# Kernel tuning notes

Hardware: AMD Instinct MI355X
Metric: run time of the kernel (lower is better)

Reference implementation:

```python
import jax, jax.numpy as jnp
import numpy as np

KMEANS_ITERS = 3   # soft-kmeans refinement iterations
TOPK = 12          # hardcoded in the torch module
EPS = 1e-8


def _gather(x, idx):
    # batched_index_select: x (b, c, m); idx (b, n, k) -> (b, c, n, k)
    return jax.vmap(lambda xb, ib: xb[:, ib])(x, idx)


def _soft_kmeans(points, cent):
    # points (b, n, c); cent (b, m, c) -> refined centroids and soft assignment weights (b, n, m)
    for _ in range(KMEANS_ITERS):
        p2 = jnp.sum(points * points, axis=-1)           # (b, n)
        c2 = jnp.sum(cent * cent, axis=-1)               # (b, m)
        logits = -(p2[:, :, None] - 2.0 * jnp.einsum('bnc,bmc->bnm', points, cent) + c2[:, None, :])
        w = jax.nn.softmax(logits, axis=-1)              # (b, n, m)
        cent = jnp.einsum('bnm,bnc->bmc', w, points) / (jnp.sum(w, axis=1)[:, :, None] + EPS)
    return cent, w


def setup_inputs():
    key = jax.random.key(0)
    k1, k2, k3 = jax.random.split(key, 3)
    b, c, H, W, k = 4, 192, 80, 80, 9
    n = H * W
    out_c = 192
    x = jax.random.normal(k1, (b, c, n, 1), dtype=jnp.float32)
    edge_index = jax.random.randint(k2, (2, b, n, k), 0, n)
    conv_w = jax.random.normal(k3, (out_c, 3 * c), dtype=jnp.float32) * (1.0 / np.sqrt(3 * c))
    conv_b = jnp.zeros((out_c,), dtype=jnp.float32)
    return {"x": x, "edge_index": edge_index, "conv_w": conv_w, "conv_b": conv_b,
            "num_centroids": 50, "H": 80, "W": 80}


def reference(x, edge_index, conv_w, conv_b, num_centroids, H, W):
    b, c, n, _ = x.shape
    xs = x[..., 0]                                        # (b, c, n)
    # initial centroids: adaptive_avg_pool2d to (5, 10); H, W chosen divisible so bins are uniform
    x_img = xs.reshape(b, c, H, W)
    init_cent = x_img.reshape(b, c, 5, H // 5, 10, W // 10).mean(axis=(3, 5)).reshape(b, c, 50)
    # edge gathers + max-relative reduction
    x_i = _gather(xs, edge_index[1])                      # (b, c, n, k)
    x_j = _gather(xs, edge_index[0])                      # (b, c, n, k)
    x_j = jnp.max(x_j - x_i, axis=-1, keepdims=True)      # (b, c, n, 1)
    # soft-kmeans centroid construction
    points = jnp.transpose(xs, (0, 2, 1))                 # (b, n, c)
    cent, weights = _soft_kmeans(points, jnp.transpose(init_cent, (0, 2, 1)))
    cent = jnp.transpose(cent, (0, 2, 1))                 # (b, c, m)
    # topk centroid routing + second gather-max stage
    _, nn_idx = jax.lax.top_k(weights, TOPK)              # (b, n, 12)
    x_jc = _gather(cent, nn_idx)                          # (b, c, n, 12)
    x_jc = jnp.max(x_jc - xs[..., None], axis=-1, keepdims=True)  # (b, c, n, 1)
    # channel-interleaved concat (matches torch stack on dim=2 then reshape to 3c)
    feat = jnp.stack([x, x_j, x_jc], axis=2).reshape(b, 3 * c, n)  # (b, 3c, n)
    # BasicConv: 1x1 conv + bias + relu (norm=None)
    out = jnp.einsum('oi,bin->bon', conv_w, feat) + conv_b[None, :, None]
    return jax.nn.relu(out)[..., None]                    # (b, out_c, n, 1)
```

## Files before the change

kernel.cpp:

```cpp
#include <hip/hip_runtime.h>
#include <hip/hip_bf16.h>
#include <math.h>

#define B_   4
#define C_   192
#define N_   6400
#define K_   9
#define M_   50
#define TK_  12
#define OC_  192
#define KC_  576
#define CH_  100
#define LSTR 53
#define TSTR 72
#define XSTR 40
#define GSTR 40
#define GPB  8

typedef __bf16 b16x8 __attribute__((ext_vector_type(8)));
typedef float f32x4 __attribute__((ext_vector_type(4)));

__device__ inline unsigned short f2b(float f) {
    union { __hip_bfloat16 h; unsigned short u; } v;
    v.h = __float2bfloat16(f);
    return v.u;
}
__device__ inline float b2f(unsigned short u) {
    union { float f; unsigned int i; } v;
    v.i = ((unsigned int)u) << 16;
    return v.f;
}
__device__ inline void up8(uint4 v, float* f) {
    unsigned int w[4] = {v.x, v.y, v.z, v.w};
#pragma unroll
    for (int i = 0; i < 4; i++) {
        f[2 * i]     = b2f((unsigned short)(w[i] & 0xffffu));
        f[2 * i + 1] = b2f((unsigned short)(w[i] >> 16));
    }
}
__device__ inline uint4 pack8(const float* f) {
    unsigned int w[4];
#pragma unroll
    for (int i = 0; i < 4; i++)
        w[i] = (unsigned int)f2b(f[2 * i]) | ((unsigned int)f2b(f[2 * i + 1]) << 16);
    uint4 v; v.x = w[0]; v.y = w[1]; v.z = w[2]; v.w = w[3];
    return v;
}

__global__ void k_transpose(const float* __restrict__ x, float* __restrict__ xt,
                            unsigned short* __restrict__ xt16,
                            unsigned short* __restrict__ xt16l,
                            const float* __restrict__ cw,
                            unsigned short* __restrict__ Wg16) {
    int tid = threadIdx.y * 32 + threadIdx.x;
    if (blockIdx.x >= 200) {
        int g = ((blockIdx.x - 200) * 24 + blockIdx.z * 6 + blockIdx.y) * 256 + tid;
        if (g < OC_ * KC_) {
            int r = g % KC_;
            Wg16[g] = f2b(cw[(g / KC_) * KC_ + (r % C_) * 3 + (r / C_)]);
        }
        return;
    }
    __shared__ float tile[32][33];
    int b = blockIdx.z;
    int p0 = blockIdx.x * 32, c0 = blockIdx.y * 32;
    int tx = threadIdx.x, ty = threadIdx.y;
    const float* xb = x + (size_t)b * C_ * N_;
    float* xtb = xt + (size_t)b * N_ * C_;
    unsigned short* xt16b = xt16 + (size_t)b * N_ * C_;
    unsigned short* xt16lb = xt16l + (size_t)b * N_ * C_;
#pragma unroll
    for (int i = 0; i < 4; i++) {
        int cc = ty + 8 * i;
        tile[cc][tx] = xb[(size_t)(c0 + cc) * N_ + p0 + tx];
    }
    __syncthreads();
#pragma unroll
    for (int i = 0; i < 4; i++) {
        int pp = ty + 8 * i;
        float v = tile[tx][pp];
        size_t o = (size_t)(p0 + pp) * C_ + c0 + tx;
        xtb[o] = v;
        unsigned short hi = f2b(v);
        xt16b[o] = hi;
        xt16lb[o] = f2b(v - b2f(hi));
    }
}

__global__ __launch_bounds__(192) void k_init_cent(const float* __restrict__ xt,
        float* __restrict__ cent, float* __restrict__ c2,
        unsigned short* __restrict__ centh, unsigned short* __restrict__ centl) {
    int m = blockIdx.x, b = blockIdx.y, c = threadIdx.x;
    if (m >= M_) {
        size_t o = ((size_t)b * 64 + m) * C_ + c;
        centh[o] = 0; centl[o] = 0;
        return;
    }
    int gy = m / 10, gx = m % 10;
    const float* xtb = xt + (size_t)b * N_ * C_;
    float s = 0.f;
    for (int yy = 0; yy < 16; yy++)
        for (int xx = 0; xx < 8; xx++) {
            int p = (gy * 16 + yy) * 80 + gx * 8 + xx;
            s += xtb[(size_t)p * C_ + c];
        }
    float v = s * (1.f / 128.f);
    cent[((size_t)b * M_ + m) * C_ + c] = v;
    size_t oh = ((size_t)b * 64 + m) * C_ + c;
    unsigned short hi = f2b(v);
    centh[oh] = hi;
    centl[oh] = f2b(v - b2f(hi));
    float q = v * v;
    __shared__ float red[3];
#pragma unroll
    for (int off = 32; off > 0; off >>= 1) q += __shfl_down(q, off, 64);
    if ((c & 63) == 0) red[c >> 6] = q;
    __syncthreads();
    if (c == 0) c2[(size_t)b * M_ + m] = red[0] + red[1] + red[2];
}

__global__ __launch_bounds__(256) void k_logits_upd(const float* __restrict__ xt,
        const unsigned short* __restrict__ xt16, const unsigned short* __restrict__ xt16l,
        const float* __restrict__ cent,
        const unsigned short* __restrict__ centh, const unsigned short* __restrict__ centl,
        const float* __restrict__ c2g,
        unsigned short* __restrict__ part, float* __restrict__ wsp,
        int* __restrict__ nn, int do_topk, int fast) {
    __shared__ alignas(16) char smem[51712];
    __shared__ float sred[256];
    float* Ac = (float*)smem;
    float* Bp = (float*)(smem + 4352);
    float* lg = (float*)(smem + 20480);
    unsigned short* lgTh = (unsigned short*)smem;
    unsigned short* lgTl = (unsigned short*)(smem + 9216);
    unsigned short* xTh = (unsigned short*)(smem + 18432);
    unsigned short* xTl = (unsigned short*)(smem + 35072);
    int b = blockIdx.y;
    int blk = blockIdx.x;
    int p0 = blk * 64;
    int tid = threadIdx.x;
    int tx = tid & 15, ty = tid >> 4;
    int lr = tid >> 2, lq = tid & 3;
    int wave = tid >> 6, lane = tid & 63;
    int m16 = lane & 15, q = lane >> 4;
    const float* xb = xt + ((size_t)b * N_ + p0) * C_;
    const unsigned short* x16b = xt16 + ((size_t)b * N_ + p0) * C_;
    const unsigned short* x16lb = xt16l + ((size_t)b * N_ + p0) * C_;
    if (fast) {
        const unsigned short* chg = centh + (size_t)b * 64 * C_;
        const unsigned short* clg = centl + (size_t)b * 64 * C_;
        f32x4 acc1[4];
#pragma unroll
        for (int i = 0; i < 4; i++) acc1[i] = (f32x4){0.f, 0.f, 0.f, 0.f};
#pragma unroll
        for (int kt = 0; kt < 6; kt++) {
            int kg = kt * 32;
            size_t xo = (size_t)(wave * 16 + m16) * C_ + kg + q * 8;
            b16x8 bh = *(const b16x8*)&x16b[xo];
            b16x8 bl = *(const b16x8*)&x16lb[xo];
#pragma unroll
            for (int mt = 0; mt < 4; mt++) {
                size_t co = (size_t)(mt * 16 + m16) * C_ + kg + q * 8;
                b16x8 ah = *(const b16x8*)&chg[co];
                b16x8 al = *(const b16x8*)&clg[co];
                acc1[mt] = __builtin_amdgcn_mfma_f32_16x16x32_bf16(ah, bh, acc1[mt], 0, 0, 0);
                acc1[mt] = __builtin_amdgcn_mfma_f32_16x16x32_bf16(ah, bl, acc1[mt], 0, 0, 0);
                acc1[mt] = __builtin_amdgcn_mfma_f32_16x16x32_bf16(al, bh, acc1[mt], 0, 0, 0);
            }
        }
#pragma unroll
        for (int mt = 0; mt < 4; mt++) {
#pragma unroll
            for (int r = 0; r < 4; r++) {
                int m = mt * 16 + q * 4 + r;
                if (m < M_) {
                    float c2v = c2g[(size_t)b * M_ + m];
                    lg[(wave * 16 + m16) * LSTR + m] = 2.f * acc1[mt][r] - c2v;
                }
            }
        }
    } else {
        const float* cb = cent + (size_t)b * M_ * C_;
        float acc[4][4];
#pragma unroll
        for (int i = 0; i < 4; i++)
#pragma unroll
            for (int j = 0; j < 4; j++) acc[i][j] = 0.f;
        for (int kt = 0; kt < 12; kt++) {
            int kg = kt * 16;
            float4 cv = make_float4(0.f, 0.f, 0.f, 0.f);
            if (lr < M_) cv = *(const float4*)&cb[(size_t)lr * C_ + kg + 4 * lq];
            float4 pv = *(const float4*)&xb[(size_t)lr * C_ + kg + 4 * lq];
            __syncthreads();
            Ac[(4 * lq + 0) * 68 + lr] = cv.x; Ac[(4 * lq + 1) * 68 + lr] = cv.y;
            Ac[(4 * lq + 2) * 68 + lr] = cv.z; Ac[(4 * lq + 3) * 68 + lr] = cv.w;
            Bp[(4 * lq + 0) * 68 + lr] = pv.x; Bp[(4 * lq + 1) * 68 + lr] = pv.y;
            Bp[(4 * lq + 2) * 68 + lr] = pv.z; Bp[(4 * lq + 3) * 68 + lr] = pv.w;
            __syncthreads();
#pragma unroll
            for (int kk = 0; kk < 16; kk++) {
                float4 a = *(const float4*)&Ac[kk * 68 + 4 * ty];
                float4 bb = *(const float4*)&Bp[kk * 68 + 4 * tx];
                acc[0][0] += a.x * bb.x; acc[0][1] += a.x * bb.y; acc[0][2] += a.x * bb.z; acc[0][3] += a.x * bb.w;
                acc[1][0] += a.y * bb.x; acc[1][1] += a.y * bb.y; acc[1][2] += a.y * bb.z; acc[1][3] += a.y * bb.w;
                acc[2][0] += a.z * bb.x; acc[2][1] += a.z * bb.y; acc[2][2] += a.z * bb.z; acc[2][3] += a.z * bb.w;
                acc[3][0] += a.w * bb.x; acc[3][1] += a.w * bb.y; acc[3][2] += a.w * bb.z; acc[3][3] += a.w * bb.w;
            }
        }
        __syncthreads();
#pragma unroll
        for (int i = 0; i < 4; i++) {
            int m = 4 * ty + i;
            if (m < M_) {
                float c2v = c2g[(size_t)b * M_ + m];
#pragma unroll
                for (int j = 0; j < 4; j++)
                    lg[(4 * tx + j) * LSTR + m] = 2.f * acc[i][j] - c2v;
            }
        }
    }
    __syncthreads();
    {
        int p = tid & 63, prt = tid >> 6;
        int m0 = prt * 13;
        int m1 = (prt == 3) ? M_ : m0 + 13;
        float* row = &lg[p * LSTR];
        float mx = -1e30f;
        for (int m = m0; m < m1; m++) mx = fmaxf(mx, row[m]);
        sred[prt * 64 + p] = mx;
        __syncthreads();
        mx = fmaxf(fmaxf(sred[p], sred[64 + p]), fmaxf(sred[128 + p], sred[192 + p]));
        float s = 0.f;
        for (int m = m0; m < m1; m++) {
            float e = expf(row[m] - mx);
            row[m] = e;
            s += e;
        }
        __syncthreads();
        sred[prt * 64 + p] = s;
        __syncthreads();
        s = sred[p] + sred[64 + p] + sred[128 + p] + sred[192 + p];
        float inv = 1.f / s;
        for (int m = m0; m < m1; m++) row[m] *= inv;
    }
    __syncthreads();
    for (int j = tid; j < 64 * 64; j += 256) {
        int m = j >> 6, p = j & 63;
        float w = (m < M_) ? lg[p * LSTR + m] : 0.f;
        unsigned short hi = f2b(w);
        lgTh[m * TSTR + p] = hi;
        lgTl[m * TSTR + p] = f2b(w - b2f(hi));
    }
    __syncthreads();
    if (do_topk && tid < 64) {
        float* row = &lg[tid * LSTR];
        int* nb = nn + ((size_t)b * N_ + p0 + tid) * TK_;
        for (int r = 0; r < TK_; r++) {
            float bv = -1.f;
            int bi = 0;
            for (int m = 0; m < M_; m++) {
                float v = row[m];
                if (v > bv) { bv = v; bi = m; }
            }
            nb[r] = bi;
            row[bi] = -1.f;
        }
    }
    f32x4 acc2[13];
#pragma unroll
    for (int i = 0; i < 13; i++) acc2[i] = (f32x4){0.f, 0.f, 0.f, 0.f};
    for (int h = 0; h < 2; h++) {
        __syncthreads();
        for (int j = tid; j < 32 * 24; j += 256) {
            int pl = j & 31, ko = (j >> 5) * 8;
            int4 vh = *(const int4*)&x16b[(size_t)(h * 32 + pl) * C_ + ko];
            int4 vl = *(const int4*)&x16lb[(size_t)(h * 32 + pl) * C_ + ko];
            const unsigned short* ph = (const unsigned short*)&vh;
            const unsigned short* pv = (const unsigned short*)&vl;
#pragma unroll
            for (int i = 0; i < 8; i++) {
                xTh[(ko + i) * XSTR + pl] = ph[i];
                xTl[(ko + i) * XSTR + pl] = pv[i];
            }
        }
        for (int j = tid; j < 32 * 16; j += 256) {
            int pl = j & 31, c = C_ + (j >> 5);
            xTh[c * XSTR + pl] = (c == C_) ? f2b(1.f) : 0;
            xTl[c * XSTR + pl] = 0;
        }
        __syncthreads();
        b16x8 ah = *(const b16x8*)&lgTh[(wave * 16 + m16) * TSTR + h * 32 + q * 8];
        b16x8 al = *(const b16x8*)&lgTl[(wave * 16 + m16) * TSTR + h * 32 + q * 8];
#pragma unroll
        for (int ct = 0; ct < 13; ct++) {
            b16x8 bh = *(const b16x8*)&xTh[(ct * 16 + m16) * XSTR + q * 8];
            b16x8 bl = *(const b16x8*)&xTl[(ct * 16 + m16) * XSTR + q * 8];
            acc2[ct] = __builtin_amdgcn_mfma_f32_16x16x32_bf16(ah, bh, acc2[ct], 0, 0, 0);
            acc2[ct] = __builtin_amdgcn_mfma_f32_16x16x32_bf16(ah, bl, acc2[ct], 0, 0, 0);
            acc2[ct] = __builtin_amdgcn_mfma_f32_16x16x32_bf16(al, bh, acc2[ct], 0, 0, 0);
        }
    }
    unsigned short* pb = part + ((size_t)b * CH_ + blk) * (size_t)(M_ * C_);
    int mbase = wave * 16 + q * 4;
#pragma unroll
    for (int ct = 0; ct < 13; ct++) {
        int c = ct * 16 + m16;
#pragma unroll
        for (int r = 0; r < 4; r++) {
            int mm = mbase + r;
            if (mm >= M_) continue;
            float v = acc2[ct][r];
            if (c < C_) pb[(size_t)mm * C_ + c] = f2b(v);
            else if (c == C_) wsp[((size_t)b * CH_ + blk) * M_ + mm] = v;
        }
    }
}

__global__ __launch_bounds__(384) void k_upd_reduce(const unsigned short* __restrict__ part,
        const float* __restrict__ wsp, float* __restrict__ cent, float* __restrict__ c2,
        unsigned short* __restrict__ cent16,
        unsigned short* __restrict__ centh, unsigned short* __restrict__ centl, int last) {
    int m = blockIdx.x, b = blockIdx.y;
    int tid = threadIdx.x;
    int c = tid % 192, g = tid / 192;
    __shared__ float pred[192];
    __shared__ float sws;
    __shared__ float red[3];
    const unsigned short* pp = part + (((size_t)b * CH_ + (size_t)g * 50) * M_ + m) * (size_t)C_ + c;
    float s = 0.f;
    for (int ch = 0; ch < 50; ch++)
        s += b2f(pp[(size_t)ch * M_ * C_]);
    if (g == 1) pred[c] = s;
    if (tid < 64) {
        float w = wsp[((size_t)b * CH_ + tid) * M_ + m];
        if (tid + 64 < CH_) w += wsp[((size_t)b * CH_ + tid + 64) * M_ + m];
#pragma unroll
        for (int off = 32; off > 0; off >>= 1) w += __shfl_down(w, off, 64);
        if (tid == 0) sws = w + 1e-8f;
    }
    __syncthreads();
    if (g == 0) {
        float v = (s + pred[c]) / sws;
        size_t o = ((size_t)b * M_ + m) * C_ + c;
        cent[o] = v;
        if (last) cent16[o] = f2b(v);
        size_t oh = ((size_t)b * 64 + m) * C_ + c;
        unsigned short hi = f2b(v);
        centh[oh] = hi;
        centl[oh] = f2b(v - b2f(hi));
        float q = v * v;
#pragma unroll
        for (int off = 32; off > 0; off >>= 1) q += __shfl_down(q, off, 64);
        if ((c & 63) == 0) red[c >> 6] = q;
    }
    __syncthreads();
    if (tid == 0) c2[(size_t)b * M_ + m] = red[0] + red[1] + red[2];
}

__global__ __launch_bounds__(192) void k_gather(const unsigned short* __restrict__ xt16,
        const unsigned short* __restrict__ cent16, const int* __restrict__ edge,
        const int* __restrict__ nn, unsigned short* __restrict__ xjt16,
        unsigned short* __restrict__ xjct16) {
    __shared__ int sidx[GPB * (2 * K_ + TK_)];
    int b = blockIdx.y;
    int p0 = blockIdx.x * GPB;
    int tid = threadIdx.x;
    for (int j = tid; j < GPB * (2 * K_ + TK_); j += 192) {
        int g = j / (2 * K_ + TK_), r = j % (2 * K_ + TK_);
        size_t base = (size_t)b * N_ + p0 + g;
        int v;
        if (r < K_) v = edge[base * K_ + r];
        else if (r < 2 * K_) v = edge[(size_t)B_ * N_ * K_ + base * K_ + (r - K_)];
        else v = nn[base * TK_ + (r - 2 * K_)];
        sidx[j] = v;
    }
    __syncthreads();
    int g = tid / 24, t = tid % 24;
    int ch0 = t * 8;
    int p = p0 + g;
    const unsigned short* xb = xt16 + (size_t)b * N_ * C_;
    const unsigned short* cb = cent16 + (size_t)b * M_ * C_;
    const int* si = &sidx[g * (2 * K_ + TK_)];
    float xv[8], ta[8], tb[8], mj[8], mc[8];
    up8(*(const uint4*)&xb[(size_t)p * C_ + ch0], xv);
#pragma unroll
    for (int e = 0; e < 8; e++) { mj[e] = -1e30f; mc[e] = -1e30f; }
#pragma unroll
    for (int kk = 0; kk < K_; kk++) {
        up8(*(const uint4*)&xb[(size_t)si[kk] * C_ + ch0], ta);
        up8(*(const uint4*)&xb[(size_t)si[K_ + kk] * C_ + ch0], tb);
#pragma unroll
        for (int e = 0; e < 8; e++) mj[e] = fmaxf(mj[e], ta[e] - tb[e]);
    }
#pragma unroll
    for (int kk = 0; kk < TK_; kk++) {
        up8(*(const uint4*)&cb[(size_t)si[2 * K_ + kk] * C_ + ch0], ta);
#pragma unroll
        for (int e = 0; e < 8; e++) mc[e] = fmaxf(mc[e], ta[e]);
    }
#pragma unroll
    for (int e = 0; e < 8; e++) mc[e] -= xv[e];
    size_t o = ((size_t)b * N_ + p) * C_ + ch0;
    *(uint4*)&xjt16[o] = pack8(mj);
    *(uint4*)&xjct16[o] = pack8(mc);
}

__global__ __launch_bounds__(256) void k_gemm(const unsigned short* __restrict__ Wg16,
        const unsigned short* __restrict__ xt16, const unsigned short* __restrict__ xjt16,
        const unsigned short* __restrict__ xjct16, const float* __restrict__ bias,
        float* __restrict__ out) {
    __shared__ short As[192 * GSTR];
    __shared__ short Bs[64 * GSTR];
    int b = blockIdx.y;
    int po = blockIdx.x * 64;
    int tid = threadIdx.x;
    int wave = tid >> 6, lane = tid & 63;
    int m16 = lane & 15, q = lane >> 4;
    const unsigned short* s0 = xt16 + (size_t)b * N_ * C_;
    const unsigned short* s1 = xjt16 + (size_t)b * N_ * C_;
    const unsigned short* s2 = xjct16 + (size_t)b * N_ * C_;
    f32x4 acc[12];
#pragma unroll
    for (int i = 0; i < 12; i++) acc[i] = (f32x4){0.f, 0.f, 0.f, 0.f};
    int brow = tid >> 2, bch = tid & 3;
    for (int kt = 0; kt < 18; kt++) {
        int kg = kt * 32;
        int prt = kg / C_, koff = kg - prt * C_;
        const unsigned short* src = (prt == 0) ? s0 : ((prt == 1) ? s1 : s2);
        int4 av[3];
#pragma unroll
        for (int t = 0; t < 3; t++) {
            int idx = t * 256 + tid;
            av[t] = *(const int4*)&Wg16[(size_t)(idx >> 2) * KC_ + kg + (idx & 3) * 8];
        }
        int4 bv = *(const int4*)&src[(size_t)(po + brow) * C_ + koff + bch * 8];
        __syncthreads();
#pragma unroll
        for (int t = 0; t < 3; t++) {
            int idx = t * 256 + tid;
            *(int4*)&As[(idx >> 2) * GSTR + (idx & 3) * 8] = av[t];
        }
        *(int4*)&Bs[brow * GSTR + bch * 8] = bv;
        __syncthreads();
        b16x8 bf = *(const b16x8*)&Bs[(wave * 16 + m16) * GSTR + q * 8];
#pragma unroll
        for (int of = 0; of < 12; of++) {
            b16x8 af = *(const b16x8*)&As[(of * 16 + m16) * GSTR + q * 8];
            acc[of] = __builtin_amdgcn_mfma_f32_16x16x32_bf16(af, bf, acc[of], 0, 0, 0);
        }
    }
    int p = po + wave * 16 + m16;
#pragma unroll
    for (int of = 0; of < 12; of++) {
        int o = of * 16 + q * 4;
        float4 bv = *(const float4*)&bias[o];
        float bia[4] = {bv.x, bv.y, bv.z, bv.w};
#pragma unroll
        for (int r = 0; r < 4; r++)
            out[((size_t)b * OC_ + o + r) * N_ + p] = fmaxf(acc[of][r] + bia[r], 0.f);
    }
}

extern "C" void kernel_launch(void* const* d_in, const int* in_sizes, int n_in,
                              void* d_out, int out_size, void* d_ws, size_t ws_size,
                              hipStream_t stream) {
    (void)in_sizes; (void)n_in; (void)out_size; (void)ws_size;
    const float* x   = (const float*)d_in[0];
    const int* edge  = (const int*)d_in[1];
    const float* cw  = (const float*)d_in[2];
    const float* cbi = (const float*)d_in[3];
    float* ws = (float*)d_ws;
    size_t o = 0;
    float* xt   = ws + o; o += (size_t)B_ * N_ * C_;
    unsigned short* xt16 = (unsigned short*)(ws + o); o += (size_t)B_ * N_ * C_ / 2;
    unsigned short* xt16l = (unsigned short*)(ws + o); o += (size_t)B_ * N_ * C_ / 2;
    unsigned short* Wg16 = (unsigned short*)(ws + o); o += (size_t)OC_ * KC_ / 2;
    float* cent = ws + o; o += (size_t)B_ * M_ * C_;
    unsigned short* cent16 = (unsigned short*)(ws + o); o += (size_t)B_ * M_ * C_ / 2;
    unsigned short* centh = (unsigned short*)(ws + o); o += (size_t)B_ * 64 * C_ / 2;
    unsigned short* centl = (unsigned short*)(ws + o); o += (size_t)B_ * 64 * C_ / 2;
    float* c2   = ws + o; o += (size_t)B_ * M_;
    unsigned short* part = (unsigned short*)(ws + o); o += (size_t)B_ * CH_ * M_ * C_ / 2;
    float* wsp  = ws + o; o += (size_t)B_ * CH_ * M_;
    int* nn = (int*)(ws + o); o += (size_t)B_ * N_ * TK_;
    unsigned short* xjt16  = (unsigned short*)(ws + o); o += (size_t)B_ * N_ * C_ / 2;
    unsigned short* xjct16 = (unsigned short*)(ws + o); o += (size_t)B_ * N_ * C_ / 2;
    float* outp = (float*)d_out;

    k_transpose<<<dim3(218, C_ / 32, B_), dim3(32, 8), 0, stream>>>(x, xt, xt16, xt16l, cw, Wg16);
    k_init_cent<<<dim3(64, B_), dim3(192), 0, stream>>>(xt, cent, c2, centh, centl);
    for (int it = 0; it < 3; it++) {
        k_logits_upd<<<dim3(CH_, B_), dim3(256), 0, stream>>>(xt, xt16, xt16l, cent,
            centh, centl, c2, part, wsp, nn, (it == 2) ? 1 : 0, (it < 2) ? 1 : 0);
        k_upd_reduce<<<dim3(M_, B_), dim3(384), 0, stream>>>(part, wsp, cent, c2,
            cent16, centh, centl, (it == 2) ? 1 : 0);
    }
    k_gather<<<dim3(N_ / GPB, B_), dim3(192), 0, stream>>>(xt16, cent16, edge, nn, xjt16, xjct16);
    k_gemm<<<dim3(N_ / 64, B_), dim3(256), 0, stream>>>(Wg16, xt16, xjt16, xjct16, cbi, outp);
}
```

Baseline: 248.3 us.

## Double thread counts in soft-kmeans logits/update and reduction kernels

The logits/update kernel moves from 256 to 512 threads. Waves split the MFMA logits tiles by point group and centroid half, and split the weighted-sum tiles across centroid tiles and column halves. The softmax reduction now uses 8 partitions of 7 centroids each. The partial-sum reduction kernel moves from 384 to 768 threads, with 4 groups of 25 chunks each. The aim is more parallelism per block, since only 400 and 200 blocks are launched, at the cost of some idle threads in the fp32 fallback path and more synchronisation traffic.

```diff
diff --git a/kernel.cpp b/kernel.cpp
--- a/kernel.cpp
+++ b/kernel.cpp
@@ -119,7 +119,7 @@
     if (c == 0) c2[(size_t)b * M_ + m] = red[0] + red[1] + red[2];
 }
 
-__global__ __launch_bounds__(256) void k_logits_upd(const float* __restrict__ xt,
+__global__ __launch_bounds__(512) void k_logits_upd(const float* __restrict__ xt,
         const unsigned short* __restrict__ xt16, const unsigned short* __restrict__ xt16l,
         const float* __restrict__ cent,
         const unsigned short* __restrict__ centh, const unsigned short* __restrict__ centl,
@@ -127,7 +127,7 @@
         unsigned short* __restrict__ part, float* __restrict__ wsp,
         int* __restrict__ nn, int do_topk, int fast) {
     __shared__ alignas(16) char smem[51712];
-    __shared__ float sred[256];
+    __shared__ float sred[512];
     float* Ac = (float*)smem;
     float* Bp = (float*)(smem + 4352);
     float* lg = (float*)(smem + 20480);
@@ -139,8 +139,8 @@
     int blk = blockIdx.x;
     int p0 = blk * 64;
     int tid = threadIdx.x;
-    int tx = tid & 15, ty = tid >> 4;
-    int lr = tid >> 2, lq = tid & 3;
+    int tx = tid & 15, ty = (tid >> 4) & 15;
+    int lr = (tid >> 2) & 63, lq = tid & 3;
     int wave = tid >> 6, lane = tid & 63;
     int m16 = lane & 15, q = lane >> 4;
     const float* xb = xt + ((size_t)b * N_ + p0) * C_;
@@ -149,33 +149,35 @@
     if (fast) {
         const unsigned short* chg = centh + (size_t)b * 64 * C_;
         const unsigned short* clg = centl + (size_t)b * 64 * C_;
-        f32x4 acc1[4];
-#pragma unroll
-        for (int i = 0; i < 4; i++) acc1[i] = (f32x4){0.f, 0.f, 0.f, 0.f};
+        int pg = wave & 3, mh = wave >> 2;
+        f32x4 acc1[2];
+#pragma unroll
+        for (int i = 0; i < 2; i++) acc1[i] = (f32x4){0.f, 0.f, 0.f, 0.f};
 #pragma unroll
         for (int kt = 0; kt < 6; kt++) {
             int kg = kt * 32;
-            size_t xo = (size_t)(wave * 16 + m16) * C_ + kg + q * 8;
+            size_t xo = (size_t)(pg * 16 + m16) * C_ + kg + q * 8;
             b16x8 bh = *(const b16x8*)&x16b[xo];
             b16x8 bl = *(const b16x8*)&x16lb[xo];
 #pragma unroll
-            for (int mt = 0; mt < 4; mt++) {
+            for (int t = 0; t < 2; t++) {
+                int mt = mh * 2 + t;
                 size_t co = (size_t)(mt * 16 + m16) * C_ + kg + q * 8;
                 b16x8 ah = *(const b16x8*)&chg[co];
                 b16x8 al = *(const b16x8*)&clg[co];
-                acc1[mt] = __builtin_amdgcn_mfma_f32_16x16x32_bf16(ah, bh, acc1[mt], 0, 0, 0);
-                acc1[mt] = __builtin_amdgcn_mfma_f32_16x16x32_bf16(ah, bl, acc1[mt], 0, 0, 0);
-                acc1[mt] = __builtin_amdgcn_mfma_f32_16x16x32_bf16(al, bh, acc1[mt], 0, 0, 0);
-            }
-        }
-#pragma unroll
-        for (int mt = 0; mt < 4; mt++) {
+                acc1[t] = __builtin_amdgcn_mfma_f32_16x16x32_bf16(ah, bh, acc1[t], 0, 0, 0);
+                acc1[t] = __builtin_amdgcn_mfma_f32_16x16x32_bf16(ah, bl, acc1[t], 0, 0, 0);
+                acc1[t] = __builtin_amdgcn_mfma_f32_16x16x32_bf16(al, bh, acc1[t], 0, 0, 0);
+            }
+        }
+#pragma unroll
+        for (int t = 0; t < 2; t++) {
 #pragma unroll
             for (int r = 0; r < 4; r++) {
-                int m = mt * 16 + q * 4 + r;
+                int m = (mh * 2 + t) * 16 + q * 4 + r;
                 if (m < M_) {
                     float c2v = c2g[(size_t)b * M_ + m];
-                    lg[(wave * 16 + m16) * LSTR + m] = 2.f * acc1[mt][r] - c2v;
+                    lg[(pg * 16 + m16) * LSTR + m] = 2.f * acc1[t][r] - c2v;
                 }
             }
         }
@@ -189,47 +191,58 @@
         for (int kt = 0; kt < 12; kt++) {
             int kg = kt * 16;
             float4 cv = make_float4(0.f, 0.f, 0.f, 0.f);
-            if (lr < M_) cv = *(const float4*)&cb[(size_t)lr * C_ + kg + 4 * lq];
-            float4 pv = *(const float4*)&xb[(size_t)lr * C_ + kg + 4 * lq];
+            float4 pv = make_float4(0.f, 0.f, 0.f, 0.f);
+            if (tid < 256) {
+                if (lr < M_) cv = *(const float4*)&cb[(size_t)lr * C_ + kg + 4 * lq];
+                pv = *(const float4*)&xb[(size_t)lr * C_ + kg + 4 * lq];
+            }
             __syncthreads();
-            Ac[(4 * lq + 0) * 68 + lr] = cv.x; Ac[(4 * lq + 1) * 68 + lr] = cv.y;
-            Ac[(4 * lq + 2) * 68 + lr] = cv.z; Ac[(4 * lq + 3) * 68 + lr] = cv.w;
-            Bp[(4 * lq + 0) * 68 + lr] = pv.x; Bp[(4 * lq + 1) * 68 + lr] = pv.y;
-            Bp[(4 * lq + 2) * 68 + lr] = pv.z; Bp[(4 * lq + 3) * 68 + lr] = pv.w;
+            if (tid < 256) {
+                Ac[(4 * lq + 0) * 68 + lr] = cv.x; Ac[(4 * lq + 1) * 68 + lr] = cv.y;
+                Ac[(4 * lq + 2) * 68 + lr] = cv.z; Ac[(4 * lq + 3) * 68 + lr] = cv.w;
+                Bp[(4 * lq + 0) * 68 + lr] = pv.x; Bp[(4 * lq + 1) * 68 + lr] = pv.y;
+                Bp[(4 * lq + 2) * 68 + lr] = pv.z; Bp[(4 * lq + 3) * 68 + lr] = pv.w;
+            }
             __syncthreads();
-#pragma unroll
-            for (int kk = 0; kk < 16; kk++) {
-                float4 a = *(const float4*)&Ac[kk * 68 + 4 * ty];
-                float4 bb = *(const float4*)&Bp[kk * 68 + 4 * tx];
-                acc[0][0] += a.x * bb.x; acc[0][1] += a.x * bb.y; acc[0][2] += a.x * bb.z; acc[0][3] += a.x * bb.w;
-                acc[1][0] += a.y * bb.x; acc[1][1] += a.y * bb.y; acc[1][2] += a.y * bb.z; acc[1][3] += a.y * bb.w;
-                acc[2][0] += a.z * bb.x; acc[2][1] += a.z * bb.y; acc[2][2] += a.z * bb.z; acc[2][3] += a.z * bb.w;
-                acc[3][0] += a.w * bb.x; acc[3][1] += a.w * bb.y; acc[3][2] += a.w * bb.z; acc[3][3] += a.w * bb.w;
-            }
-        }
-        __syncthreads();
-#pragma unroll
-        for (int i = 0; i < 4; i++) {
-            int m = 4 * ty + i;
-            if (m < M_) {
-                float c2v = c2g[(size_t)b * M_ + m];
-#pragma unroll
-                for (int j = 0; j < 4; j++)
-                    lg[(4 * tx + j) * LSTR + m] = 2.f * acc[i][j] - c2v;
+            if (tid < 256) {
+#pragma unroll
+                for (int kk = 0; kk < 16; kk++) {
+                    float4 a = *(const float4*)&Ac[kk * 68 + 4 * ty];
+                    float4 bb = *(const float4*)&Bp[kk * 68 + 4 * tx];
+                    acc[0][0] += a.x * bb.x; acc[0][1] += a.x * bb.y; acc[0][2] += a.x * bb.z; acc[0][3] += a.x * bb.w;
+                    acc[1][0] += a.y * bb.x; acc[1][1] += a.y * bb.y; acc[1][2] += a.y * bb.z; acc[1][3] += a.y * bb.w;
+                    acc[2][0] += a.z * bb.x; acc[2][1] += a.z * bb.y; acc[2][2] += a.z * bb.z; acc[2][3] += a.z * bb.w;
+                    acc[3][0] += a.w * bb.x; acc[3][1] += a.w * bb.y; acc[3][2] += a.w * bb.z; acc[3][3] += a.w * bb.w;
+                }
+            }
+        }
+        __syncthreads();
+        if (tid < 256) {
+#pragma unroll
+            for (int i = 0; i < 4; i++) {
+                int m = 4 * ty + i;
+                if (m < M_) {
+                    float c2v = c2g[(size_t)b * M_ + m];
+#pragma unroll
+                    for (int j = 0; j < 4; j++)
+                        lg[(4 * tx + j) * LSTR + m] = 2.f * acc[i][j] - c2v;
+                }
             }
         }
     }
     __syncthreads();
     {
         int p = tid & 63, prt = tid >> 6;
-        int m0 = prt * 13;
-        int m1 = (prt == 3) ? M_ : m0 + 13;
+        int m0 = prt * 7;
+        int m1 = (m0 + 7 > M_) ? M_ : m0 + 7;
         float* row = &lg[p * LSTR];
         float mx = -1e30f;
         for (int m = m0; m < m1; m++) mx = fmaxf(mx, row[m]);
         sred[prt * 64 + p] = mx;
         __syncthreads();
-        mx = fmaxf(fmaxf(sred[p], sred[64 + p]), fmaxf(sred[128 + p], sred[192 + p]));
+        mx = -1e30f;
+#pragma unroll
+        for (int k = 0; k < 8; k++) mx = fmaxf(mx, sred[k * 64 + p]);
         float s = 0.f;
         for (int m = m0; m < m1; m++) {
             float e = expf(row[m] - mx);
@@ -239,12 +252,14 @@
         __syncthreads();
         sred[prt * 64 + p] = s;
         __syncthreads();
-        s = sred[p] + sred[64 + p] + sred[128 + p] + sred[192 + p];
+        s = 0.f;
+#pragma unroll
+        for (int k = 0; k < 8; k++) s += sred[k * 64 + p];
         float inv = 1.f / s;
         for (int m = m0; m < m1; m++) row[m] *= inv;
     }
     __syncthreads();
-    for (int j = tid; j < 64 * 64; j += 256) {
+    for (int j = tid; j < 64 * 64; j += 512) {
         int m = j >> 6, p = j & 63;
         float w = (m < M_) ? lg[p * LSTR + m] : 0.f;
         unsigned short hi = f2b(w);
@@ -266,12 +281,13 @@
             row[bi] = -1.f;
         }
     }
-    f32x4 acc2[13];
-#pragma unroll
-    for (int i = 0; i < 13; i++) acc2[i] = (f32x4){0.f, 0.f, 0.f, 0.f};
+    int mt2 = wave >> 1, cbase = (wave & 1) * 7;
+    f32x4 acc2[7];
+#pragma unroll
+    for (int i = 0; i < 7; i++) acc2[i] = (f32x4){0.f, 0.f, 0.f, 0.f};
     for (int h = 0; h < 2; h++) {
         __syncthreads();
-        for (int j = tid; j < 32 * 24; j += 256) {
+        for (int j = tid; j < 32 * 24; j += 512) {
             int pl = j & 31, ko = (j >> 5) * 8;
             int4 vh = *(const int4*)&x16b[(size_t)(h * 32 + pl) * C_ + ko];
             int4 vl = *(const int4*)&x16lb[(size_t)(h * 32 + pl) * C_ + ko];
@@ -283,54 +299,58 @@
                 xTl[(ko + i) * XSTR + pl] = pv[i];
             }
         }
-        for (int j = tid; j < 32 * 16; j += 256) {
+        for (int j = tid; j < 32 * 16; j += 512) {
             int pl = j & 31, c = C_ + (j >> 5);
             xTh[c * XSTR + pl] = (c == C_) ? f2b(1.f) : 0;
             xTl[c * XSTR + pl] = 0;
         }
         __syncthreads();
-        b16x8 ah = *(const b16x8*)&lgTh[(wave * 16 + m16) * TSTR + h * 32 + q * 8];
-        b16x8 al = *(const b16x8*)&lgTl[(wave * 16 + m16) * TSTR + h * 32 + q * 8];
-#pragma unroll
-        for (int ct = 0; ct < 13; ct++) {
+        b16x8 ah = *(const b16x8*)&lgTh[(mt2 * 16 + m16) * TSTR + h * 32 + q * 8];
+        b16x8 al = *(const b16x8*)&lgTl[(mt2 * 16 + m16) * TSTR + h * 32 + q * 8];
+#pragma unroll
+        for (int ci = 0; ci < 7; ci++) {
+            int ct = cbase + ci;
+            if (ct >= 13) continue;
             b16x8 bh = *(const b16x8*)&xTh[(ct * 16 + m16) * XSTR + q * 8];
             b16x8 bl = *(const b16x8*)&xTl[(ct * 16 + m16) * XSTR + q * 8];
-            acc2[ct] = __builtin_amdgcn_mfma_f32_16x16x32_bf16(ah, bh, acc2[ct], 0, 0, 0);
-            acc2[ct] = __builtin_amdgcn_mfma_f32_16x16x32_bf16(ah, bl, acc2[ct], 0, 0, 0);
-            acc2[ct] = __builtin_amdgcn_mfma_f32_16x16x32_bf16(al, bh, acc2[ct], 0, 0, 0);
+            acc2[ci] = __builtin_amdgcn_mfma_f32_16x16x32_bf16(ah, bh, acc2[ci], 0, 0, 0);
+            acc2[ci] = __builtin_amdgcn_mfma_f32_16x16x32_bf16(ah, bl, acc2[ci], 0, 0, 0);
+            acc2[ci] = __builtin_amdgcn_mfma_f32_16x16x32_bf16(al, bh, acc2[ci], 0, 0, 0);
         }
     }
     unsigned short* pb = part + ((size_t)b * CH_ + blk) * (size_t)(M_ * C_);
-    int mbase = wave * 16 + q * 4;
-#pragma unroll
-    for (int ct = 0; ct < 13; ct++) {
+    int mbase = mt2 * 16 + q * 4;
+#pragma unroll
+    for (int ci = 0; ci < 7; ci++) {
+        int ct = cbase + ci;
+        if (ct >= 13) continue;
         int c = ct * 16 + m16;
 #pragma unroll
         for (int r = 0; r < 4; r++) {
             int mm = mbase + r;
             if (mm >= M_) continue;
-            float v = acc2[ct][r];
+            float v = acc2[ci][r];
             if (c < C_) pb[(size_t)mm * C_ + c] = f2b(v);
             else if (c == C_) wsp[((size_t)b * CH_ + blk) * M_ + mm] = v;
         }
     }
 }
 
-__global__ __launch_bounds__(384) void k_upd_reduce(const unsigned short* __restrict__ part,
+__global__ __launch_bounds__(768) void k_upd_reduce(const unsigned short* __restrict__ part,
         const float* __restrict__ wsp, float* __restrict__ cent, float* __restrict__ c2,
         unsigned short* __restrict__ cent16,
         unsigned short* __restrict__ centh, unsigned short* __restrict__ centl, int last) {
     int m = blockIdx.x, b = blockIdx.y;
     int tid = threadIdx.x;
     int c = tid % 192, g = tid / 192;
-    __shared__ float pred[192];
+    __shared__ float pred[3][192];
     __shared__ float sws;
     __shared__ float red[3];
-    const unsigned short* pp = part + (((size_t)b * CH_ + (size_t)g * 50) * M_ + m) * (size_t)C_ + c;
+    const unsigned short* pp = part + (((size_t)b * CH_ + (size_t)g * 25) * M_ + m) * (size_t)C_ + c;
     float s = 0.f;
-    for (int ch = 0; ch < 50; ch++)
+    for (int ch = 0; ch < 25; ch++)
         s += b2f(pp[(size_t)ch * M_ * C_]);
-    if (g == 1) pred[c] = s;
+    if (g) pred[g - 1][c] = s;
     if (tid < 64) {
         float w = wsp[((size_t)b * CH_ + tid) * M_ + m];
         if (tid + 64 < CH_) w += wsp[((size_t)b * CH_ + tid + 64) * M_ + m];
@@ -340,7 +360,7 @@
     }
     __syncthreads();
     if (g == 0) {
-        float v = (s + pred[c]) / sws;
+        float v = (s + pred[0][c] + pred[1][c] + pred[2][c]) / sws;
         size_t o = ((size_t)b * M_ + m) * C_ + c;
         cent[o] = v;
         if (last) cent16[o] = f2b(v);
@@ -490,9 +510,9 @@
     k_transpose<<<dim3(218, C_ / 32, B_), dim3(32, 8), 0, stream>>>(x, xt, xt16, xt16l, cw, Wg16);
     k_init_cent<<<dim3(64, B_), dim3(192), 0, stream>>>(xt, cent, c2, centh, centl);
     for (int it = 0; it < 3; it++) {
-        k_logits_upd<<<dim3(CH_, B_), dim3(256), 0, stream>>>(xt, xt16, xt16l, cent,
+        k_logits_upd<<<dim3(CH_, B_), dim3(512), 0, stream>>>(xt, xt16, xt16l, cent,
             centh, centl, c2, part, wsp, nn, (it == 2) ? 1 : 0, (it < 2) ? 1 : 0);
-        k_upd_reduce<<<dim3(M_, B_), dim3(384), 0, stream>>>(part, wsp, cent, c2,
+        k_upd_reduce<<<dim3(M_, B_), dim3(768), 0, stream>>>(part, wsp, cent, c2,
             cent16, centh, centl, (it == 2) ? 1 : 0);
     }
     k_gather<<<dim3(N_ / GPB, B_), dim3(192), 0, stream>>>(xt16, cent16, edge, nn, xjt16, xjct16);
```

Result: no change. 246.5 us (median of 2 runs) (-0.7%).
